# Performance work log

Measured on AMD Instinct MI355X. Metric: run time of the kernel, lower is better.

The kernel has to match this reference:

```python
import jax, jax.numpy as jnp
import numpy as np

EPS = 1e-12  # torch F.normalize eps

def rmsnorm(x, g, dim):
    # F.normalize(x, dim=-1) * sqrt(dim) * g  (g is a learned scalar)
    n = jnp.maximum(jnp.linalg.norm(x, axis=-1, keepdims=True), EPS)
    return x / n * (dim ** 0.5) * g

def modulate(x, scale, shift):
    # x: (B,T,D); scale/shift: (B,D)
    return x * (1.0 + scale[:, None, :]) + shift[:, None, :]

def setup_inputs() -> dict:
    key = jax.random.key(0)
    ks = jax.random.split(key, 12)
    B, T, D, H = 8, 1024, 1024, 16
    Dm = 4 * D
    s = 0.02
    inp = {
        'x': jax.random.normal(ks[0], (B, T, D), jnp.float32),
        'c': jax.random.normal(ks[1], (B, D), jnp.float32),
        'g1': jnp.ones((1,), jnp.float32),
        'g2': jnp.ones((1,), jnp.float32),
        'gq': jnp.ones((1,), jnp.float32),
        'gk': jnp.ones((1,), jnp.float32),
        'Wqkv': jax.random.normal(ks[2], (3 * D, D), jnp.float32) * s,
        'bqkv': jnp.zeros((3 * D,), jnp.float32),
        'Wproj': jax.random.normal(ks[3], (D, D), jnp.float32) * s,
        'bproj': jnp.zeros((D,), jnp.float32),
        'Wfc1': jax.random.normal(ks[4], (Dm, D), jnp.float32) * s,
        'bfc1': jnp.zeros((Dm,), jnp.float32),
        'Wfc2': jax.random.normal(ks[5], (D, Dm), jnp.float32) * s,
        'bfc2': jnp.zeros((D,), jnp.float32),
        'Wada': jax.random.normal(ks[6], (6 * D, D), jnp.float32) * s,
        'bada': jnp.zeros((6 * D,), jnp.float32),
    }
    return inp

def reference(x, c, g1, g2, gq, gk, Wqkv, bqkv, Wproj, bproj,
              Wfc1, bfc1, Wfc2, bfc2, Wada, bada):
    B, T, D = x.shape
    H = 16
    hd = D // H

    # adaLN modulation: SiLU -> Linear -> chunk 6 along last dim
    ada = jax.nn.silu(c) @ Wada.T + bada  # (B, 6D)
    shift_msa, scale_msa, gate_msa, shift_mlp, scale_mlp, gate_mlp = jnp.split(ada, 6, axis=-1)

    # --- attention branch ---
    h = modulate(rmsnorm(x, g1, D), scale_msa, shift_msa)  # (B,T,D)
    qkv = h @ Wqkv.T + bqkv  # (B,T,3D)
    qkv = qkv.reshape(B, T, 3, H, hd).transpose(2, 0, 3, 1, 4)  # (3,B,H,T,hd)
    q, k, v = qkv[0], qkv[1], qkv[2]
    q = rmsnorm(q, gq, hd) * (hd ** -0.5)
    k = rmsnorm(k, gk, hd)
    attn = jax.nn.softmax(jnp.einsum('bhqd,bhkd->bhqk', q, k), axis=-1)
    o = jnp.einsum('bhqk,bhkd->bhqd', attn, v)  # (B,H,T,hd)
    o = o.transpose(0, 2, 1, 3).reshape(B, T, D)
    o = o @ Wproj.T + bproj
    x = x + gate_msa[:, None, :] * o

    # --- MLP branch ---
    h = modulate(rmsnorm(x, g2, D), scale_mlp, shift_mlp)
    h = jax.nn.gelu(h @ Wfc1.T + bfc1, approximate=True)
    h = h @ Wfc2.T + bfc2
    x = x + gate_mlp[:, None, :] * h
    return x
```

## Files before the change

### kernel.cpp

```cpp
#include <hip/hip_runtime.h>
#include <hip/hip_bf16.h>
#include <math.h>

typedef __bf16 bf16x8 __attribute__((ext_vector_type(8)));
typedef __bf16 bf16x4 __attribute__((ext_vector_type(4)));
typedef float  f32x4  __attribute__((ext_vector_type(4)));

#define DEV static __device__ __forceinline__

DEV unsigned short f2bf(float f) {
    unsigned u = __builtin_bit_cast(unsigned, f);
    u += 0x7fffu + ((u >> 16) & 1u);
    return (unsigned short)(u >> 16);
}
DEV float bf2f(unsigned short u) {
    unsigned x = ((unsigned)u) << 16;
    return __builtin_bit_cast(float, x);
}

__global__ void k_cvtall(const float* __restrict__ a, const float* __restrict__ b,
                         const float* __restrict__ c, const float* __restrict__ d,
                         unsigned short* __restrict__ oa, unsigned short* __restrict__ ob,
                         unsigned short* __restrict__ oc, unsigned short* __restrict__ od) {
    size_t i = (size_t)blockIdx.x * 1024 + threadIdx.x * 4;
    const float* src; unsigned short* dst; size_t off;
    if (i < 3145728)      { src = a; dst = oa; off = i; }
    else if (i < 4194304) { src = b; dst = ob; off = i - 3145728; }
    else if (i < 8388608) { src = c; dst = oc; off = i - 4194304; }
    else                  { src = d; dst = od; off = i - 8388608; }
    float4 v = *(const float4*)(src + off);
    ushort4 o;
    o.x = f2bf(v.x); o.y = f2bf(v.y); o.z = f2bf(v.z); o.w = f2bf(v.w);
    *(ushort4*)(dst + off) = o;
}

__global__ void k_ada(const float* __restrict__ c, const float* __restrict__ Wada,
                      const float* __restrict__ bada, float* __restrict__ ada) {
    __shared__ float sc[1024];
    int b = blockIdx.x;
    int tid = threadIdx.x;
    for (int k = tid; k < 1024; k += 256) {
        float x = c[b * 1024 + k];
        sc[k] = x / (1.f + __expf(-x));
    }
    __syncthreads();
    int wid = tid >> 6, lane = tid & 63;
    int n = blockIdx.y * 4 + wid;
    const float* wr = Wada + (size_t)n * 1024;
    float acc = 0.f;
    #pragma unroll
    for (int k = 0; k < 1024; k += 64) acc += sc[k + lane] * wr[k + lane];
    #pragma unroll
    for (int o = 32; o; o >>= 1) acc += __shfl_xor(acc, o);
    if (lane == 0) ada[b * 6144 + n] = acc + bada[n];
}

__global__ void k_norm_mod(const float* __restrict__ x, const float* __restrict__ ada,
                           const float* __restrict__ g, unsigned short* __restrict__ h,
                           int shift_off, int scale_off) {
    int row = blockIdx.x;
    int b = row >> 10;
    int tid = threadIdx.x;
    float4 v = *(const float4*)(x + (size_t)row * 1024 + tid * 4);
    float ss = v.x * v.x + v.y * v.y + v.z * v.z + v.w * v.w;
    #pragma unroll
    for (int o = 32; o; o >>= 1) ss += __shfl_xor(ss, o);
    __shared__ float red[4];
    int wid = tid >> 6, lane = tid & 63;
    if (lane == 0) red[wid] = ss;
    __syncthreads();
    float nrm = sqrtf(red[0] + red[1] + red[2] + red[3]);
    float f = g[0] * 32.f / fmaxf(nrm, 1e-12f);
    float4 s4 = *(const float4*)(ada + b * 6144 + scale_off + tid * 4);
    float4 h4 = *(const float4*)(ada + b * 6144 + shift_off + tid * 4);
    ushort4 o;
    o.x = f2bf(v.x * f * (1.f + s4.x) + h4.x);
    o.y = f2bf(v.y * f * (1.f + s4.y) + h4.y);
    o.z = f2bf(v.z * f * (1.f + s4.z) + h4.z);
    o.w = f2bf(v.w * f * (1.f + s4.w) + h4.w);
    *(ushort4*)(h + (size_t)row * 1024 + tid * 4) = o;
}

template <int EPI>
__global__ __launch_bounds__(256, 4)
void k_gemm5(const unsigned short* __restrict__ A, const unsigned short* __restrict__ Bw,
             const float* __restrict__ bias, int N, int K, int gridM, int gridN, int Kc,
             unsigned short* __restrict__ outH) {
    __shared__ unsigned short lA[128 * 64];
    __shared__ unsigned short lB[128 * 64];
    int tid = threadIdx.x;
    int wid = tid >> 6, lane = tid & 63;
    int li = lane & 15, lg = lane >> 4;
    int bid = blockIdx.x;
    int mb = bid % gridM;
    int nb = (bid / gridM) % gridN;
    int sp = bid / (gridM * gridN);
    int m0 = mb * 128, n0 = nb * 128;
    int k0 = sp * Kc;
    int wr = (wid >> 1) * 64, wc = (wid & 1) * 64;

    int trow = tid >> 3;
    int gcol = ((tid & 7) ^ (trow & 7)) * 8;
    int sl0 = (lg ^ (li & 7)) * 8;
    int sl1 = ((4 + lg) ^ (li & 7)) * 8;

    f32x4 acc[4][4] = {};

    for (int kk = 0; kk < Kc; kk += 64) {
        #pragma unroll
        for (int l = 0; l < 4; ++l) {
            int row = l * 32 + trow;
            const unsigned short* ga = A  + (size_t)(m0 + row) * K + k0 + kk + gcol;
            const unsigned short* gb = Bw + (size_t)(n0 + row) * K + k0 + kk + gcol;
            unsigned short* la = lA + (l * 256 + wid * 64) * 8;
            unsigned short* lb = lB + (l * 256 + wid * 64) * 8;
            __builtin_amdgcn_global_load_lds((const __attribute__((address_space(1))) void*)ga,
                                             (__attribute__((address_space(3))) void*)la, 16, 0, 0);
            __builtin_amdgcn_global_load_lds((const __attribute__((address_space(1))) void*)gb,
                                             (__attribute__((address_space(3))) void*)lb, 16, 0, 0);
        }
        __syncthreads();
        bf16x8 af[4], bfr[4];
        #pragma unroll
        for (int i = 0; i < 4; ++i)
            af[i] = *(const bf16x8*)(lA + (wr + i * 16 + li) * 64 + sl0);
        #pragma unroll
        for (int j = 0; j < 4; ++j)
            bfr[j] = *(const bf16x8*)(lB + (wc + j * 16 + li) * 64 + sl0);
        #pragma unroll
        for (int i = 0; i < 4; ++i)
            #pragma unroll
            for (int j = 0; j < 4; ++j)
                acc[i][j] = __builtin_amdgcn_mfma_f32_16x16x32_bf16(af[i], bfr[j], acc[i][j], 0, 0, 0);
        #pragma unroll
        for (int i = 0; i < 4; ++i)
            af[i] = *(const bf16x8*)(lA + (wr + i * 16 + li) * 64 + sl1);
        #pragma unroll
        for (int j = 0; j < 4; ++j)
            bfr[j] = *(const bf16x8*)(lB + (wc + j * 16 + li) * 64 + sl1);
        #pragma unroll
        for (int i = 0; i < 4; ++i)
            #pragma unroll
            for (int j = 0; j < 4; ++j)
                acc[i][j] = __builtin_amdgcn_mfma_f32_16x16x32_bf16(af[i], bfr[j], acc[i][j], 0, 0, 0);
        __syncthreads();
    }

    int rb4 = lg * 4;
    size_t poff = (size_t)sp * ((size_t)8192 * N);
    #pragma unroll
    for (int i = 0; i < 4; ++i) {
        #pragma unroll
        for (int j = 0; j < 4; ++j) {
            #pragma unroll
            for (int r = 0; r < 4; ++r) {
                int row = m0 + wr + i * 16 + rb4 + r;
                int col = n0 + wc + j * 16 + li;
                if (EPI == 0) {
                    outH[(size_t)row * N + col] = f2bf(acc[i][j][r] + bias[col]);
                } else if (EPI == 2) {
                    float vv = acc[i][j][r] + bias[col];
                    float a2 = 0.7978845608f * (vv + 0.044715f * vv * vv * vv);
                    float e = __expf(-2.f * fabsf(a2));
                    float th = copysignf((1.f - e) / (1.f + e), a2);
                    outH[(size_t)row * N + col] = f2bf(0.5f * vv * (1.f + th));
                } else {
                    outH[poff + (size_t)row * N + col] = f2bf(acc[i][j][r]);
                }
            }
        }
    }
}

__global__ void k_fix_norm(const float* __restrict__ x, const unsigned short* __restrict__ P,
                           const float* __restrict__ bias, const float* __restrict__ ada,
                           const float* __restrict__ g2, float* __restrict__ out,
                           unsigned short* __restrict__ h2) {
    int row = blockIdx.x, b = row >> 10, tid = threadIdx.x;
    int c = tid * 4;
    size_t base = (size_t)row * 1024 + c;
    ushort4 p0 = *(const ushort4*)(P + base);
    ushort4 p1 = *(const ushort4*)(P + 8388608 + base);
    float4 xv = *(const float4*)(x + base);
    float4 bi = *(const float4*)(bias + c);
    float4 gt = *(const float4*)(ada + b * 6144 + 2048 + c);
    float4 v;
    v.x = xv.x + gt.x * (bf2f(p0.x) + bf2f(p1.x) + bi.x);
    v.y = xv.y + gt.y * (bf2f(p0.y) + bf2f(p1.y) + bi.y);
    v.z = xv.z + gt.z * (bf2f(p0.z) + bf2f(p1.z) + bi.z);
    v.w = xv.w + gt.w * (bf2f(p0.w) + bf2f(p1.w) + bi.w);
    *(float4*)(out + base) = v;
    float ss = v.x * v.x + v.y * v.y + v.z * v.z + v.w * v.w;
    #pragma unroll
    for (int o = 32; o; o >>= 1) ss += __shfl_xor(ss, o);
    __shared__ float red[4];
    int wid = tid >> 6, lane = tid & 63;
    if (lane == 0) red[wid] = ss;
    __syncthreads();
    float nrm = sqrtf(red[0] + red[1] + red[2] + red[3]);
    float f = g2[0] * 32.f / fmaxf(nrm, 1e-12f);
    float4 sc = *(const float4*)(ada + b * 6144 + 4096 + c);
    float4 sh = *(const float4*)(ada + b * 6144 + 3072 + c);
    ushort4 o;
    o.x = f2bf(v.x * f * (1.f + sc.x) + sh.x);
    o.y = f2bf(v.y * f * (1.f + sc.y) + sh.y);
    o.z = f2bf(v.z * f * (1.f + sc.z) + sh.z);
    o.w = f2bf(v.w * f * (1.f + sc.w) + sh.w);
    *(ushort4*)(h2 + base) = o;
}

__global__ void k_fixf(const unsigned short* __restrict__ P, const float* __restrict__ bias,
                       const float* __restrict__ ada, float* __restrict__ out) {
    int row = blockIdx.x, b = row >> 10, tid = threadIdx.x;
    int c = tid * 4;
    size_t base = (size_t)row * 1024 + c;
    ushort4 p0 = *(const ushort4*)(P + base);
    ushort4 p1 = *(const ushort4*)(P + 8388608 + base);
    float4 xv = *(const float4*)(out + base);
    float4 bi = *(const float4*)(bias + c);
    float4 gt = *(const float4*)(ada + b * 6144 + 5120 + c);
    float4 v;
    v.x = xv.x + gt.x * (bf2f(p0.x) + bf2f(p1.x) + bi.x);
    v.y = xv.y + gt.y * (bf2f(p0.y) + bf2f(p1.y) + bi.y);
    v.z = xv.z + gt.z * (bf2f(p0.z) + bf2f(p1.z) + bi.z);
    v.w = xv.w + gt.w * (bf2f(p0.w) + bf2f(p1.w) + bi.w);
    *(float4*)(out + base) = v;
}

__global__ __launch_bounds__(256)
void k_vt(const unsigned short* __restrict__ qkv, unsigned short* __restrict__ Vtg) {
    __shared__ unsigned short vt[64 * 72];
    int bh = blockIdx.x;
    int b = bh >> 4, h = bh & 15;
    int t0 = blockIdx.y * 64;
    int tid = threadIdx.x;
    int row = tid >> 2, part = tid & 3;
    size_t rbase = ((size_t)(b * 1024 + t0 + row)) * 3072 + 2048 + h * 64 + part * 16;
    uint4 u0 = *(const uint4*)(qkv + rbase);
    uint4 u1 = *(const uint4*)(qkv + rbase + 8);
    const unsigned* pu = (const unsigned*)&u0;
    #pragma unroll
    for (int j = 0; j < 4; ++j) {
        vt[(part * 16 + 2*j)     * 72 + row] = (unsigned short)(pu[j] & 0xffff);
        vt[(part * 16 + 2*j + 1) * 72 + row] = (unsigned short)(pu[j] >> 16);
    }
    pu = (const unsigned*)&u1;
    #pragma unroll
    for (int j = 0; j < 4; ++j) {
        vt[(part * 16 + 8 + 2*j)     * 72 + row] = (unsigned short)(pu[j] & 0xffff);
        vt[(part * 16 + 8 + 2*j + 1) * 72 + row] = (unsigned short)(pu[j] >> 16);
    }
    __syncthreads();
    int d = tid >> 2, seg = tid & 3;
    uint4 w0 = *(const uint4*)(vt + d * 72 + seg * 16);
    uint4 w1 = *(const uint4*)(vt + d * 72 + seg * 16 + 8);
    size_t vdst = (size_t)bh * 65536 + (size_t)d * 1024 + t0 + seg * 16;
    *(uint4*)(Vtg + vdst)     = w0;
    *(uint4*)(Vtg + vdst + 8) = w1;
}

__global__ __launch_bounds__(256)
void k_attn2(const unsigned short* __restrict__ qkv,
             const unsigned short* __restrict__ Vtg,
             const float* __restrict__ gq, const float* __restrict__ gk,
             unsigned short* __restrict__ outp) {
    __shared__ unsigned short Kt[128 * 64];
    __shared__ unsigned short Vl[64 * 136];
    __shared__ float normv[128];
    int bh = blockIdx.x;
    int b = bh >> 4, h = bh & 15;
    int t0 = blockIdx.y * 64;
    int tid = threadIdx.x, wid = tid >> 6, lane = tid & 63;
    int li = lane & 15, lg = lane >> 4;
    const size_t bh64k = (size_t)bh * 65536;

    bf16x8 q0, q1;
    {
        int qrow = b * 1024 + t0 + wid * 16 + li;
        const unsigned short* Qg = qkv + (size_t)qrow * 3072 + h * 64 + lg * 8;
        bf16x8 r0 = *(const bf16x8*)Qg;
        bf16x8 r1 = *(const bf16x8*)(Qg + 32);
        float ssq = 0.f;
        #pragma unroll
        for (int j = 0; j < 8; ++j) {
            float a = (float)r0[j], bb = (float)r1[j];
            ssq += a * a + bb * bb;
        }
        ssq += __shfl_xor(ssq, 16);
        ssq += __shfl_xor(ssq, 32);
        float qs = gq[0] / fmaxf(sqrtf(ssq), 1e-12f);
        #pragma unroll
        for (int j = 0; j < 8; ++j) {
            q0[j] = (__bf16)((float)r0[j] * qs);
            q1[j] = (__bf16)((float)r1[j] * qs);
        }
    }
    float gk8 = 8.f * gk[0];
    f32x4 oacc[4] = {};
    float den = 0.f;

    for (int kt = 0; kt < 8; ++kt) {
        __syncthreads();
        #pragma unroll
        for (int i = 0; i < 4; ++i) {
            int s = i * 256 + tid;
            int r = s >> 3, c16 = s & 7;
            const unsigned short* src = qkv + (size_t)(b * 1024 + kt * 128 + r) * 3072
                                        + 1024 + h * 64 + ((c16 ^ (r & 7)) * 8);
            unsigned short* dst = Kt + i * 2048 + wid * 512;
            __builtin_amdgcn_global_load_lds((const __attribute__((address_space(1))) void*)src,
                                             (__attribute__((address_space(3))) void*)dst, 16, 0, 0);
        }
        #pragma unroll
        for (int i = 0; i < 4; ++i) {
            int s = i * 256 + tid;
            int d = s >> 4, k16 = s & 15;
            uint4 v = *(const uint4*)(Vtg + bh64k + (size_t)d * 1024 + kt * 128 + k16 * 8);
            *(uint4*)(Vl + d * 136 + k16 * 8) = v;
        }
        __syncthreads();
        {
            int r = tid >> 1, hh = tid & 1;
            float ss = 0.f;
            #pragma unroll
            for (int j = 0; j < 4; ++j) {
                bf16x8 kv = *(const bf16x8*)(Kt + r * 64 + (((hh * 4 + j) ^ (r & 7)) * 8));
                #pragma unroll
                for (int u = 0; u < 8; ++u) { float a = (float)kv[u]; ss += a * a; }
            }
            ss += __shfl_xor(ss, 1);
            if (!hh) normv[r] = gk8 / fmaxf(sqrtf(ss), 1e-12f);
        }
        __syncthreads();

        f32x4 st[8];
        #pragma unroll
        for (int f = 0; f < 8; ++f) {
            int row = f * 16 + li;
            bf16x8 a0 = *(const bf16x8*)(Kt + row * 64 + ((lg       ^ (row & 7)) * 8));
            bf16x8 a1 = *(const bf16x8*)(Kt + row * 64 + (((4 + lg) ^ (row & 7)) * 8));
            f32x4 s = {};
            s = __builtin_amdgcn_mfma_f32_16x16x32_bf16(a0, q0, s, 0, 0, 0);
            s = __builtin_amdgcn_mfma_f32_16x16x32_bf16(a1, q1, s, 0, 0, 0);
            f32x4 nv = *(const f32x4*)(normv + f * 16 + lg * 4);
            f32x4 e;
            e[0] = __expf(s[0] * nv[0]); e[1] = __expf(s[1] * nv[1]);
            e[2] = __expf(s[2] * nv[2]); e[3] = __expf(s[3] * nv[3]);
            den += e[0] + e[1] + e[2] + e[3];
            st[f] = e;
        }
        #pragma unroll
        for (int ks = 0; ks < 4; ++ks) {
            f32x4 e0 = st[2 * ks], e1 = st[2 * ks + 1];
            bf16x8 pa;
            pa[0] = (__bf16)e0[0]; pa[1] = (__bf16)e0[1]; pa[2] = (__bf16)e0[2]; pa[3] = (__bf16)e0[3];
            pa[4] = (__bf16)e1[0]; pa[5] = (__bf16)e1[1]; pa[6] = (__bf16)e1[2]; pa[7] = (__bf16)e1[3];
            #pragma unroll
            for (int df = 0; df < 4; ++df) {
                const unsigned short* vp = Vl + (df * 16 + li) * 136 + ks * 32 + lg * 4;
                bf16x4 v0 = *(const bf16x4*)vp;
                bf16x4 v1 = *(const bf16x4*)(vp + 16);
                bf16x8 vb = __builtin_shufflevector(v0, v1, 0, 1, 2, 3, 4, 5, 6, 7);
                oacc[df] = __builtin_amdgcn_mfma_f32_16x16x32_bf16(pa, vb, oacc[df], 0, 0, 0);
            }
        }
    }
    den += __shfl_xor(den, 16);
    den += __shfl_xor(den, 32);

    #pragma unroll
    for (int r2 = 0; r2 < 4; ++r2) {
        float dm = __shfl(den, lg * 4 + r2);
        float inv = 1.f / dm;
        int t = t0 + wid * 16 + lg * 4 + r2;
        #pragma unroll
        for (int df = 0; df < 4; ++df) {
            int col = h * 64 + df * 16 + li;
            outp[((size_t)(b * 1024 + t)) * 1024 + col] = f2bf(oacc[df][r2] * inv);
        }
    }
}

extern "C" void kernel_launch(void* const* d_in, const int* in_sizes, int n_in,
                              void* d_out, int out_size, void* d_ws, size_t ws_size,
                              hipStream_t stream) {
    const float* x     = (const float*)d_in[0];
    const float* c     = (const float*)d_in[1];
    const float* g1    = (const float*)d_in[2];
    const float* g2    = (const float*)d_in[3];
    const float* gq    = (const float*)d_in[4];
    const float* gk    = (const float*)d_in[5];
    const float* Wqkv  = (const float*)d_in[6];
    const float* bqkv  = (const float*)d_in[7];
    const float* Wproj = (const float*)d_in[8];
    const float* bproj = (const float*)d_in[9];
    const float* Wfc1  = (const float*)d_in[10];
    const float* bfc1  = (const float*)d_in[11];
    const float* Wfc2  = (const float*)d_in[12];
    const float* bfc2  = (const float*)d_in[13];
    const float* Wada  = (const float*)d_in[14];
    const float* bada  = (const float*)d_in[15];
    float* out = (float*)d_out;

    char* ws = (char*)d_ws;
    unsigned short* wqkv_bf = (unsigned short*)ws; ws += (size_t)3072 * 1024 * 2;
    unsigned short* wproj_bf= (unsigned short*)ws; ws += (size_t)1024 * 1024 * 2;
    unsigned short* wfc1_bf = (unsigned short*)ws; ws += (size_t)4096 * 1024 * 2;
    unsigned short* wfc2_bf = (unsigned short*)ws; ws += (size_t)4096 * 1024 * 2;
    float* ada = (float*)ws;                       ws += (size_t)8 * 6144 * 4;
    unsigned short* hbuf = (unsigned short*)ws;    ws += (size_t)8192 * 1024 * 2;
    unsigned short* qkvb16 = (unsigned short*)ws;  ws += (size_t)8192 * 3072 * 2;
    unsigned short* Vtg = (unsigned short*)ws;     ws += (size_t)8192 * 64 * 16 * 2;
    unsigned short* Pbuf = (unsigned short*)ws;    ws += (size_t)2 * 8192 * 1024 * 2;
    unsigned short* fc1out = qkvb16;

    k_cvtall<<<12288, 256, 0, stream>>>(Wqkv, Wproj, Wfc1, Wfc2,
                                        wqkv_bf, wproj_bf, wfc1_bf, wfc2_bf);
    k_ada<<<dim3(8, 1536), 256, 0, stream>>>(c, Wada, bada, ada);
    k_norm_mod<<<8192, 256, 0, stream>>>(x, ada, g1, hbuf, 0, 1024);
    k_gemm5<0><<<1536, 256, 0, stream>>>(hbuf, wqkv_bf, bqkv, 3072, 1024, 64, 24, 1024, qkvb16);
    k_vt<<<dim3(128, 16), 256, 0, stream>>>(qkvb16, Vtg);
    k_attn2<<<dim3(128, 16), 256, 0, stream>>>(qkvb16, Vtg, gq, gk, hbuf);
    k_gemm5<4><<<1024, 256, 0, stream>>>(hbuf, wproj_bf, bproj, 1024, 1024, 64, 8, 512, Pbuf);
    k_fix_norm<<<8192, 256, 0, stream>>>(x, Pbuf, bproj, ada, g2, out, hbuf);
    k_gemm5<2><<<2048, 256, 0, stream>>>(hbuf, wfc1_bf, bfc1, 4096, 1024, 64, 32, 1024, fc1out);
    k_gemm5<4><<<1024, 256, 0, stream>>>(fc1out, wfc2_bf, bfc2, 1024, 4096, 64, 8, 2048, Pbuf);
    k_fixf<<<8192, 256, 0, stream>>>(Pbuf, bfc2, ada, out);
}
```

Before: 399.6 us.

## Fuse per-head Q/K RMS normalization into QKV GEMM epilogue

Adds a new QKV GEMM epilogue that applies the per-head RMS normalization and gain scaling to Q and K tiles before storing them as bf16, using cross-lane shuffles over each 64-wide head. The attention kernel then reads pre-normalized Q and K. This drops its per-tile K-norm pass, one barrier and the score rescale. It removes redundant K-norm work, since each K tile was renormalized by all 16 query blocks, at the cost of a heavier GEMM epilogue with more registers and shuffles.

```diff
diff --git a/kernel.cpp b/kernel.cpp
--- a/kernel.cpp
+++ b/kernel.cpp
@@ -85,7 +85,8 @@
 __global__ __launch_bounds__(256, 4)
 void k_gemm5(const unsigned short* __restrict__ A, const unsigned short* __restrict__ Bw,
              const float* __restrict__ bias, int N, int K, int gridM, int gridN, int Kc,
-             unsigned short* __restrict__ outH) {
+             unsigned short* __restrict__ outH,
+             const float* __restrict__ gq, const float* __restrict__ gk) {
     __shared__ unsigned short lA[128 * 64];
     __shared__ unsigned short lB[128 * 64];
     int tid = threadIdx.x;
@@ -148,6 +149,51 @@
 
     int rb4 = lg * 4;
     size_t poff = (size_t)sp * ((size_t)8192 * N);
+    if (EPI == 5) {
+        int typ = n0 >> 10;
+        if (typ == 2) {
+            #pragma unroll
+            for (int i = 0; i < 4; ++i)
+                #pragma unroll
+                for (int j = 0; j < 4; ++j)
+                    #pragma unroll
+                    for (int r = 0; r < 4; ++r) {
+                        int row = m0 + wr + i * 16 + rb4 + r;
+                        int col = n0 + wc + j * 16 + li;
+                        outH[(size_t)row * N + col] = f2bf(acc[i][j][r] + bias[col]);
+                    }
+        } else {
+            float gsc = (typ == 0) ? gq[0] : 8.f * gk[0];
+            #pragma unroll
+            for (int i = 0; i < 4; ++i) {
+                #pragma unroll
+                for (int j = 0; j < 4; ++j)
+                    #pragma unroll
+                    for (int r = 0; r < 4; ++r)
+                        acc[i][j][r] += bias[n0 + wc + j * 16 + li];
+                float scl[4];
+                #pragma unroll
+                for (int r = 0; r < 4; ++r) {
+                    float s = acc[i][0][r] * acc[i][0][r] + acc[i][1][r] * acc[i][1][r]
+                            + acc[i][2][r] * acc[i][2][r] + acc[i][3][r] * acc[i][3][r];
+                    s += __shfl_xor(s, 1);
+                    s += __shfl_xor(s, 2);
+                    s += __shfl_xor(s, 4);
+                    s += __shfl_xor(s, 8);
+                    scl[r] = gsc / fmaxf(sqrtf(s), 1e-12f);
+                }
+                #pragma unroll
+                for (int j = 0; j < 4; ++j)
+                    #pragma unroll
+                    for (int r = 0; r < 4; ++r) {
+                        int row = m0 + wr + i * 16 + rb4 + r;
+                        int col = n0 + wc + j * 16 + li;
+                        outH[(size_t)row * N + col] = f2bf(acc[i][j][r] * scl[r]);
+                    }
+            }
+        }
+        return;
+    }
     #pragma unroll
     for (int i = 0; i < 4; ++i) {
         #pragma unroll
@@ -260,13 +306,11 @@
 }
 
 __global__ __launch_bounds__(256)
-void k_attn2(const unsigned short* __restrict__ qkv,
+void k_attn3(const unsigned short* __restrict__ qkv,
              const unsigned short* __restrict__ Vtg,
-             const float* __restrict__ gq, const float* __restrict__ gk,
              unsigned short* __restrict__ outp) {
     __shared__ unsigned short Kt[128 * 64];
     __shared__ unsigned short Vl[64 * 136];
-    __shared__ float normv[128];
     int bh = blockIdx.x;
     int b = bh >> 4, h = bh & 15;
     int t0 = blockIdx.y * 64;
@@ -278,24 +322,9 @@
     {
         int qrow = b * 1024 + t0 + wid * 16 + li;
         const unsigned short* Qg = qkv + (size_t)qrow * 3072 + h * 64 + lg * 8;
-        bf16x8 r0 = *(const bf16x8*)Qg;
-        bf16x8 r1 = *(const bf16x8*)(Qg + 32);
-        float ssq = 0.f;
-        #pragma unroll
-        for (int j = 0; j < 8; ++j) {
-            float a = (float)r0[j], bb = (float)r1[j];
-            ssq += a * a + bb * bb;
-        }
-        ssq += __shfl_xor(ssq, 16);
-        ssq += __shfl_xor(ssq, 32);
-        float qs = gq[0] / fmaxf(sqrtf(ssq), 1e-12f);
-        #pragma unroll
-        for (int j = 0; j < 8; ++j) {
-            q0[j] = (__bf16)((float)r0[j] * qs);
-            q1[j] = (__bf16)((float)r1[j] * qs);
-        }
-    }
-    float gk8 = 8.f * gk[0];
+        q0 = *(const bf16x8*)Qg;
+        q1 = *(const bf16x8*)(Qg + 32);
+    }
     f32x4 oacc[4] = {};
     float den = 0.f;
 
@@ -319,19 +348,6 @@
             *(uint4*)(Vl + d * 136 + k16 * 8) = v;
         }
         __syncthreads();
-        {
-            int r = tid >> 1, hh = tid & 1;
-            float ss = 0.f;
-            #pragma unroll
-            for (int j = 0; j < 4; ++j) {
-                bf16x8 kv = *(const bf16x8*)(Kt + r * 64 + (((hh * 4 + j) ^ (r & 7)) * 8));
-                #pragma unroll
-                for (int u = 0; u < 8; ++u) { float a = (float)kv[u]; ss += a * a; }
-            }
-            ss += __shfl_xor(ss, 1);
-            if (!hh) normv[r] = gk8 / fmaxf(sqrtf(ss), 1e-12f);
-        }
-        __syncthreads();
 
         f32x4 st[8];
         #pragma unroll
@@ -342,10 +358,9 @@
             f32x4 s = {};
             s = __builtin_amdgcn_mfma_f32_16x16x32_bf16(a0, q0, s, 0, 0, 0);
             s = __builtin_amdgcn_mfma_f32_16x16x32_bf16(a1, q1, s, 0, 0, 0);
-            f32x4 nv = *(const f32x4*)(normv + f * 16 + lg * 4);
             f32x4 e;
-            e[0] = __expf(s[0] * nv[0]); e[1] = __expf(s[1] * nv[1]);
-            e[2] = __expf(s[2] * nv[2]); e[3] = __expf(s[3] * nv[3]);
+            e[0] = __expf(s[0]); e[1] = __expf(s[1]);
+            e[2] = __expf(s[2]); e[3] = __expf(s[3]);
             den += e[0] + e[1] + e[2] + e[3];
             st[f] = e;
         }
@@ -418,12 +433,16 @@
                                         wqkv_bf, wproj_bf, wfc1_bf, wfc2_bf);
     k_ada<<<dim3(8, 1536), 256, 0, stream>>>(c, Wada, bada, ada);
     k_norm_mod<<<8192, 256, 0, stream>>>(x, ada, g1, hbuf, 0, 1024);
-    k_gemm5<0><<<1536, 256, 0, stream>>>(hbuf, wqkv_bf, bqkv, 3072, 1024, 64, 24, 1024, qkvb16);
+    k_gemm5<5><<<1536, 256, 0, stream>>>(hbuf, wqkv_bf, bqkv, 3072, 1024, 64, 24, 1024,
+                                         qkvb16, gq, gk);
     k_vt<<<dim3(128, 16), 256, 0, stream>>>(qkvb16, Vtg);
-    k_attn2<<<dim3(128, 16), 256, 0, stream>>>(qkvb16, Vtg, gq, gk, hbuf);
-    k_gemm5<4><<<1024, 256, 0, stream>>>(hbuf, wproj_bf, bproj, 1024, 1024, 64, 8, 512, Pbuf);
+    k_attn3<<<dim3(128, 16), 256, 0, stream>>>(qkvb16, Vtg, hbuf);
+    k_gemm5<4><<<1024, 256, 0, stream>>>(hbuf, wproj_bf, bproj, 1024, 1024, 64, 8, 512,
+                                         Pbuf, nullptr, nullptr);
     k_fix_norm<<<8192, 256, 0, stream>>>(x, Pbuf, bproj, ada, g2, out, hbuf);
-    k_gemm5<2><<<2048, 256, 0, stream>>>(hbuf, wfc1_bf, bfc1, 4096, 1024, 64, 32, 1024, fc1out);
-    k_gemm5<4><<<1024, 256, 0, stream>>>(fc1out, wfc2_bf, bfc2, 1024, 4096, 64, 8, 2048, Pbuf);
+    k_gemm5<2><<<2048, 256, 0, stream>>>(hbuf, wfc1_bf, bfc1, 4096, 1024, 64, 32, 1024,
+                                         fc1out, nullptr, nullptr);
+    k_gemm5<4><<<1024, 256, 0, stream>>>(fc1out, wfc2_bf, bfc2, 1024, 4096, 64, 8, 2048,
+                                         Pbuf, nullptr, nullptr);
     k_fixf<<<8192, 256, 0, stream>>>(Pbuf, bfc2, ada, out);
 }
```

Measured after the change: 389.5 us. 2.5% less time.
